# Kernel tuning notes

Hardware: AMD Instinct MI355X
Metric: run time of the kernel (lower is better)

The kernel has to match this reference:

```python
import jax, jax.numpy as jnp
import numpy as np

N, L2, C = 4096, 49, 128   # lmax=6 -> (lmax+1)**2 = 49
RES = 18                   # grid resolution (beta, alpha)


def setup_inputs() -> dict:
    key = jax.random.key(0)
    k1, k2, k3 = jax.random.split(key, 3)
    inputs = jax.random.normal(k1, (N, L2, C), dtype=jnp.float32)
    # Stand-ins for the precomputed spherical-harmonic transform matrices
    # (to_grid_mat / from_grid_mat), shape (res_beta, res_alpha, (lmax+1)**2).
    W_to = jax.random.normal(k2, (RES, RES, L2), dtype=jnp.float32) / jnp.sqrt(jnp.float32(L2))
    W_from = jax.random.normal(k3, (RES, RES, L2), dtype=jnp.float32) / jnp.sqrt(jnp.float32(RES * RES))
    return {"inputs": inputs, "W_to": W_to, "W_from": W_from}


def reference(inputs, W_to, W_from):
    # to_grid: coefficients -> real-space S2 grid  (n, beta, alpha, c)
    grid = jnp.einsum('bai,nic->nbac', W_to, inputs)
    # elementwise self tensor product on the grid
    grid = grid * grid
    # from_grid: project back to spherical-harmonic coefficients (n, i, c)
    outputs = jnp.einsum('bai,nbac->nic', W_from, grid)
    return outputs
```

## Files before the change

### kernel.cpp

```cpp
#include <hip/hip_runtime.h>


#define NN    4096
#define L2D   49
#define CCH   128
#define GTOT  324
#define MT1P  22
#define KC2   11

typedef __attribute__((ext_vector_type(8))) short bf16x8;
typedef __attribute__((ext_vector_type(4))) float f32x4;

#define WT_SHORTS (MT1P * 2 * 64 * 8)
#define WF_SHORTS (4 * KC2 * 64 * 8)

__device__ __forceinline__ short f2bf(float f) {
    union { float f; unsigned u; } x; x.f = f;
    return (short)((x.u + 0x7fffu + ((x.u >> 16) & 1u)) >> 16);
}

__global__ void prep_w_kernel(const float* __restrict__ Wt,
                              const float* __restrict__ Wf,
                              short* __restrict__ WtF,
                              short* __restrict__ WfF)
{
    int idx = blockIdx.x * 256 + threadIdx.x;
    if (idx < WT_SHORTS) {
        int j = idx & 7, lane = (idx >> 3) & 63, kcx = (idx >> 9) & 1, mt = idx >> 10;
        int g = mt * 16 + (lane & 15);
        int i = kcx * 32 + (lane >> 4) * 8 + j;
        WtF[idx] = f2bf((g < GTOT && i < L2D) ? Wt[g * L2D + i] : 0.0f);
    } else if (idx < WT_SHORTS + WF_SHORTS) {
        int e = idx - WT_SHORTS;
        int j = e & 7, lane = (e >> 3) & 63, t = e >> 9;
        int kc2 = t % KC2, it = t / KC2;
        int i = it * 16 + (lane & 15);
        int g = kc2 * 32 + (j >> 2) * 16 + (lane >> 4) * 4 + (j & 3);
        WfF[e] = f2bf((g < GTOT && i < L2D) ? Wf[g * L2D + i] : 0.0f);
    }
}

__global__ __launch_bounds__(256, 3)
void stp_mfma2_kernel(const float* __restrict__ inp,
                      const short* __restrict__ WtF,
                      const short* __restrict__ WfF,
                      float* __restrict__ out)
{
    const int tid  = threadIdx.x;
    const int lane = tid & 63;
    const int wave = tid >> 6;
    const int lm   = lane & 15;
    const int quad = lane >> 4;

    const int task = blockIdx.x * 4 + wave;
    const int n    = task >> 1;
    const int h    = task & 1;

    const float* __restrict__ Xn = inp + (size_t)n * (L2D * CCH);

    bf16x8 Bx[4][2];
    #pragma unroll
    for (int t = 0; t < 4; ++t) {
        const int c = h * 64 + t * 16 + lm;
        #pragma unroll
        for (int kcx = 0; kcx < 2; ++kcx) {
            bf16x8 b;
            #pragma unroll
            for (int j = 0; j < 8; ++j) {
                const int i = kcx * 32 + quad * 8 + j;
                float v = 0.0f;
                if (i < L2D) v = Xn[i * CCH + c];
                b[j] = f2bf(v);
            }
            Bx[t][kcx] = b;
        }
    }

    f32x4 acc2[4][4];
    #pragma unroll
    for (int it = 0; it < 4; ++it)
        #pragma unroll
        for (int t = 0; t < 4; ++t)
            acc2[it][t] = (f32x4){0.0f, 0.0f, 0.0f, 0.0f};

    #pragma unroll 1
    for (int kc2 = 0; kc2 < KC2; ++kc2) {
        bf16x8 Wtf[2][2];
        #pragma unroll
        for (int tt = 0; tt < 2; ++tt)
            #pragma unroll
            for (int kcx = 0; kcx < 2; ++kcx)
                Wtf[tt][kcx] = *(const bf16x8*)&WtF[(((2 * kc2 + tt) * 2 + kcx) * 64 + lane) * 8];
        bf16x8 Wff[4];
        #pragma unroll
        for (int it = 0; it < 4; ++it)
            Wff[it] = *(const bf16x8*)&WfF[((it * KC2 + kc2) * 64 + lane) * 8];

        #pragma unroll
        for (int t = 0; t < 4; ++t) {
            bf16x8 Bg;
            #pragma unroll
            for (int tt = 0; tt < 2; ++tt) {
                f32x4 gacc = (f32x4){0.0f, 0.0f, 0.0f, 0.0f};
                gacc = __builtin_amdgcn_mfma_f32_16x16x32_bf16(Wtf[tt][0], Bx[t][0], gacc, 0, 0, 0);
                gacc = __builtin_amdgcn_mfma_f32_16x16x32_bf16(Wtf[tt][1], Bx[t][1], gacc, 0, 0, 0);
                #pragma unroll
                for (int r = 0; r < 4; ++r)
                    Bg[tt * 4 + r] = f2bf(gacc[r] * gacc[r]);
            }
            #pragma unroll
            for (int it = 0; it < 4; ++it)
                acc2[it][t] = __builtin_amdgcn_mfma_f32_16x16x32_bf16(Wff[it], Bg, acc2[it][t], 0, 0, 0);
        }
    }

    float* __restrict__ On = out + (size_t)n * (L2D * CCH);
    #pragma unroll
    for (int it = 0; it < 4; ++it) {
        #pragma unroll
        for (int t = 0; t < 4; ++t) {
            const int c = h * 64 + t * 16 + lm;
            #pragma unroll
            for (int r = 0; r < 4; ++r) {
                const int i = it * 16 + quad * 4 + r;
                if (i < L2D) On[i * CCH + c] = acc2[it][t][r];
            }
        }
    }
}

extern "C" void kernel_launch(void* const* d_in, const int* in_sizes, int n_in,
                              void* d_out, int out_size, void* d_ws, size_t ws_size,
                              hipStream_t stream) {
    const float* inp = (const float*)d_in[0];
    const float* Wt  = (const float*)d_in[1];
    const float* Wf  = (const float*)d_in[2];
    float* out = (float*)d_out;

    short* WtF = (short*)d_ws;
    short* WfF = WtF + WT_SHORTS;

    const int prep_threads = WT_SHORTS + WF_SHORTS;
    prep_w_kernel<<<(prep_threads + 255) / 256, 256, 0, stream>>>(Wt, Wf, WtF, WfF);
    stp_mfma2_kernel<<<2048, 256, 0, stream>>>(inp, WtF, WfF, out);
}
```

Measured before the change: 215.0 us.

## Stage transform weights in LDS and make persistent 1024-thread blocks loop over samples

```diff
diff --git a/kernel.cpp b/kernel.cpp
--- a/kernel.cpp
+++ b/kernel.cpp
@@ -13,10 +13,17 @@
 
 #define WT_SHORTS (MT1P * 2 * 64 * 8)
 #define WF_SHORTS (4 * KC2 * 64 * 8)
+#define W_SHORTS  (WT_SHORTS + WF_SHORTS)
 
 __device__ __forceinline__ short f2bf(float f) {
     union { float f; unsigned u; } x; x.f = f;
     return (short)((x.u + 0x7fffu + ((x.u >> 16) & 1u)) >> 16);
+}
+
+__device__ __forceinline__ unsigned cvtpk(float lo, float hi) {
+    unsigned r;
+    asm("v_cvt_pk_bf16_f32 %0, %1, %2" : "=v"(r) : "v"(lo), "v"(hi));
+    return r;
 }
 
 __global__ void prep_w_kernel(const float* __restrict__ Wt,
@@ -40,90 +47,106 @@
     }
 }
 
-__global__ __launch_bounds__(256, 3)
-void stp_mfma2_kernel(const float* __restrict__ inp,
-                      const short* __restrict__ WtF,
-                      const short* __restrict__ WfF,
+__global__ __launch_bounds__(1024, 4)
+void stp_mfma3_kernel(const float* __restrict__ inp,
+                      const short* __restrict__ Wbase,
                       float* __restrict__ out)
 {
-    const int tid  = threadIdx.x;
+    __shared__ __attribute__((aligned(16))) short sW[W_SHORTS];
+
+    const int tid = threadIdx.x;
+
+    {
+        const uint4* __restrict__ src = (const uint4*)Wbase;
+        uint4* dst = (uint4*)sW;
+        #pragma unroll
+        for (int e = 0; e < 6; ++e) {
+            int idx = tid + e * 1024;
+            if (idx < W_SHORTS / 8) dst[idx] = src[idx];
+        }
+    }
+    __syncthreads();
+
     const int lane = tid & 63;
     const int wave = tid >> 6;
     const int lm   = lane & 15;
     const int quad = lane >> 4;
+    const int q    = wave & 3;
+    const int nw   = wave >> 2;
 
-    const int task = blockIdx.x * 4 + wave;
-    const int n    = task >> 1;
-    const int h    = task & 1;
+    const short* sWt = sW;
+    const short* sWf = sW + WT_SHORTS;
 
-    const float* __restrict__ Xn = inp + (size_t)n * (L2D * CCH);
+    for (int rep = 0; rep < 4; ++rep) {
+        const int n = blockIdx.x * 16 + rep * 4 + nw;
+        const float* __restrict__ Xn = inp + (size_t)n * (L2D * CCH);
 
-    bf16x8 Bx[4][2];
-    #pragma unroll
-    for (int t = 0; t < 4; ++t) {
-        const int c = h * 64 + t * 16 + lm;
+        bf16x8 Bx[2][2];
         #pragma unroll
-        for (int kcx = 0; kcx < 2; ++kcx) {
-            bf16x8 b;
+        for (int t = 0; t < 2; ++t) {
+            const int c = q * 32 + t * 16 + lm;
             #pragma unroll
-            for (int j = 0; j < 8; ++j) {
-                const int i = kcx * 32 + quad * 8 + j;
-                float v = 0.0f;
-                if (i < L2D) v = Xn[i * CCH + c];
-                b[j] = f2bf(v);
+            for (int kcx = 0; kcx < 2; ++kcx) {
+                union { bf16x8 v; unsigned u[4]; } b;
+                #pragma unroll
+                for (int p = 0; p < 4; ++p) {
+                    const int i0 = kcx * 32 + quad * 8 + 2 * p;
+                    float v0 = (i0     < L2D) ? Xn[(i0    ) * CCH + c] : 0.0f;
+                    float v1 = (i0 + 1 < L2D) ? Xn[(i0 + 1) * CCH + c] : 0.0f;
+                    b.u[p] = cvtpk(v0, v1);
+                }
+                Bx[t][kcx] = b.v;
             }
-            Bx[t][kcx] = b;
         }
-    }
 
-    f32x4 acc2[4][4];
-    #pragma unroll
-    for (int it = 0; it < 4; ++it)
-        #pragma unroll
-        for (int t = 0; t < 4; ++t)
-            acc2[it][t] = (f32x4){0.0f, 0.0f, 0.0f, 0.0f};
-
-    #pragma unroll 1
-    for (int kc2 = 0; kc2 < KC2; ++kc2) {
-        bf16x8 Wtf[2][2];
-        #pragma unroll
-        for (int tt = 0; tt < 2; ++tt)
-            #pragma unroll
-            for (int kcx = 0; kcx < 2; ++kcx)
-                Wtf[tt][kcx] = *(const bf16x8*)&WtF[(((2 * kc2 + tt) * 2 + kcx) * 64 + lane) * 8];
-        bf16x8 Wff[4];
+        f32x4 acc2[4][2];
         #pragma unroll
         for (int it = 0; it < 4; ++it)
-            Wff[it] = *(const bf16x8*)&WfF[((it * KC2 + kc2) * 64 + lane) * 8];
+            #pragma unroll
+            for (int t = 0; t < 2; ++t)
+                acc2[it][t] = (f32x4){0.0f, 0.0f, 0.0f, 0.0f};
 
-        #pragma unroll
-        for (int t = 0; t < 4; ++t) {
-            bf16x8 Bg;
+        #pragma unroll 1
+        for (int kc2 = 0; kc2 < KC2; ++kc2) {
+            bf16x8 Wtf[2][2];
             #pragma unroll
-            for (int tt = 0; tt < 2; ++tt) {
-                f32x4 gacc = (f32x4){0.0f, 0.0f, 0.0f, 0.0f};
-                gacc = __builtin_amdgcn_mfma_f32_16x16x32_bf16(Wtf[tt][0], Bx[t][0], gacc, 0, 0, 0);
-                gacc = __builtin_amdgcn_mfma_f32_16x16x32_bf16(Wtf[tt][1], Bx[t][1], gacc, 0, 0, 0);
+            for (int tt = 0; tt < 2; ++tt)
                 #pragma unroll
-                for (int r = 0; r < 4; ++r)
-                    Bg[tt * 4 + r] = f2bf(gacc[r] * gacc[r]);
-            }
+                for (int kcx = 0; kcx < 2; ++kcx)
+                    Wtf[tt][kcx] = *(const bf16x8*)&sWt[(((2 * kc2 + tt) * 2 + kcx) * 64 + lane) * 8];
+            bf16x8 Wff[4];
             #pragma unroll
             for (int it = 0; it < 4; ++it)
-                acc2[it][t] = __builtin_amdgcn_mfma_f32_16x16x32_bf16(Wff[it], Bg, acc2[it][t], 0, 0, 0);
+                Wff[it] = *(const bf16x8*)&sWf[((it * KC2 + kc2) * 64 + lane) * 8];
+
+            #pragma unroll
+            for (int t = 0; t < 2; ++t) {
+                union { bf16x8 v; unsigned u[4]; } bg;
+                #pragma unroll
+                for (int tt = 0; tt < 2; ++tt) {
+                    f32x4 g = (f32x4){0.0f, 0.0f, 0.0f, 0.0f};
+                    g = __builtin_amdgcn_mfma_f32_16x16x32_bf16(Wtf[tt][0], Bx[t][0], g, 0, 0, 0);
+                    g = __builtin_amdgcn_mfma_f32_16x16x32_bf16(Wtf[tt][1], Bx[t][1], g, 0, 0, 0);
+                    bg.u[tt * 2 + 0] = cvtpk(g[0] * g[0], g[1] * g[1]);
+                    bg.u[tt * 2 + 1] = cvtpk(g[2] * g[2], g[3] * g[3]);
+                }
+                #pragma unroll
+                for (int it = 0; it < 4; ++it)
+                    acc2[it][t] = __builtin_amdgcn_mfma_f32_16x16x32_bf16(Wff[it], bg.v, acc2[it][t], 0, 0, 0);
+            }
         }
-    }
 
-    float* __restrict__ On = out + (size_t)n * (L2D * CCH);
-    #pragma unroll
-    for (int it = 0; it < 4; ++it) {
+        float* __restrict__ On = out + (size_t)n * (L2D * CCH);
         #pragma unroll
-        for (int t = 0; t < 4; ++t) {
-            const int c = h * 64 + t * 16 + lm;
+        for (int it = 0; it < 4; ++it) {
             #pragma unroll
-            for (int r = 0; r < 4; ++r) {
-                const int i = it * 16 + quad * 4 + r;
-                if (i < L2D) On[i * CCH + c] = acc2[it][t][r];
+            for (int t = 0; t < 2; ++t) {
+                const int c = q * 32 + t * 16 + lm;
+                #pragma unroll
+                for (int r = 0; r < 4; ++r) {
+                    const int i = it * 16 + quad * 4 + r;
+                    if (i < L2D) On[i * CCH + c] = acc2[it][t][r];
+                }
             }
         }
     }
@@ -142,5 +165,5 @@
 
     const int prep_threads = WT_SHORTS + WF_SHORTS;
     prep_w_kernel<<<(prep_threads + 255) / 256, 256, 0, stream>>>(Wt, Wf, WtF, WfF);
-    stp_mfma2_kernel<<<2048, 256, 0, stream>>>(inp, WtF, WfF, out);
+    stp_mfma3_kernel<<<256, 1024, 0, stream>>>(inp, (const short*)WtF, out);
 }
```

After: 232.0 us. 1.08x slower.
